# Optimization experiments

Hardware: AMD Instinct MI355X
Metric: run time of the kernel (lower is better)

## Reference

```python
import jax, jax.numpy as jnp
import numpy as np

NUM_POINTS = 1024  # K from init_kwargs


def setup_inputs() -> dict:
    key = jax.random.key(0)
    # [B, N, C]: xyz in channels 0:3, extra features (e.g. normals) in 3:6
    points = jax.random.normal(key, (16, 131072, 6), dtype=jnp.float32)
    return {"points": points}


def _fps_indices(xyz, K):
    """Iterative farthest-point sampling. xyz: [B, N, 3] -> idx [B, K] int32.
    random_start_point in the torch source is replaced by a fixed start (index 0)
    for determinism; the algorithm is otherwise identical."""
    B, N, _ = xyz.shape
    start = jnp.zeros((B,), dtype=jnp.int32)
    init_dists = jnp.full((B, N), jnp.inf, dtype=xyz.dtype)

    def step(carry, _):
        dists, last = carry
        # gather last selected point: [B, 1, 3]
        p = jnp.take_along_axis(xyz, last[:, None, None], axis=1)
        d = jnp.sum((xyz - p) ** 2, axis=-1)          # [B, N]
        dists = jnp.minimum(dists, d)                 # running min dist to selected set
        nxt = jnp.argmax(dists, axis=-1).astype(jnp.int32)
        return (dists, nxt), nxt

    (_, _), rest = jax.lax.scan(step, (init_dists, start), None, length=K - 1)
    # rest: [K-1, B] -> assemble [B, K] with the start index first
    idx = jnp.concatenate([start[:, None], rest.T], axis=1)
    return idx


def reference(points):
    xyz = points[:, :, :3].astype(jnp.float32)
    idx = _fps_indices(xyz, NUM_POINTS)               # [B, K]
    # masked_gather (all indices valid): gather rows along point dim
    out = jnp.take_along_axis(points, idx[:, :, None], axis=1)  # [B, K, C]
    return out
```

## Files before the change

### kernel.cpp

```cpp
#include <hip/hip_runtime.h>

#define BATCH 16
#define NPTS  131072
#define NCH   6
#define KSEL  1024
#define MBLK  16
#define TPB   256
#define CHUNK (NPTS / MBLK)
#define PPT   (CHUNK / TPB)
#define NWAVE (TPB / 64)
#define ROT   2


extern "C" __global__ __launch_bounds__(TPB)
void fps_kernel(const float* __restrict__ pts, float* __restrict__ out,
                unsigned long long* __restrict__ pub)
{
#pragma clang fp contract(off)
    __shared__ float              s_wd[NWAVE];
    __shared__ int                s_wi[NWAVE];
    __shared__ unsigned long long s_key[MBLK];

    const int b    = blockIdx.x % BATCH;
    const int m    = blockIdx.x / BATCH;
    const int tid  = threadIdx.x;
    const int base = m * CHUNK;
    const float* __restrict__ pb = pts + (size_t)b * NPTS * NCH;

    float xr[PPT], yr[PPT], zr[PPT], dmin[PPT];
#pragma unroll
    for (int i = 0; i < PPT; ++i) {
        const float* p = pb + (size_t)(base + tid + i * TPB) * NCH;
        xr[i]   = p[0];
        yr[i]   = p[1];
        zr[i]   = p[2];
        dmin[i] = __builtin_inff();
    }

    if (m == 0 && tid < NCH) out[(size_t)b * KSEL * NCH + tid] = pb[tid];

    float px = pb[0], py = pb[1], pz = pb[2];

    for (int k = 1; k < KSEL; ++k) {
        float bd = -1.0f;
        int   bj = 0;
#pragma unroll
        for (int i = 0; i < PPT; ++i) {
            float dx = __fsub_rn(xr[i], px);
            float dy = __fsub_rn(yr[i], py);
            float dz = __fsub_rn(zr[i], pz);
            float d  = __fadd_rn(__fadd_rn(__fmul_rn(dx, dx),
                                           __fmul_rn(dy, dy)),
                                 __fmul_rn(dz, dz));
            float dm = dmin[i];
            dm = (d < dm) ? d : dm;
            dmin[i] = dm;
            if (dm > bd) { bd = dm; bj = tid + i * TPB; }
        }

        for (int off = 32; off > 0; off >>= 1) {
            float od = __shfl_down(bd, off);
            int   oj = __shfl_down(bj, off);
            if (od > bd || (od == bd && oj < bj)) { bd = od; bj = oj; }
        }
        if ((tid & 63) == 0) {
            const int w = tid >> 6;
            s_wd[w] = bd; s_wi[w] = bj;
        }
        __syncthreads();

        unsigned long long* slot =
            pub + ((size_t)b * ROT + (size_t)(k & (ROT - 1))) * MBLK;

        if (tid == 0) {
            float fd = s_wd[0]; int fi = s_wi[0];
#pragma unroll
            for (int w = 1; w < NWAVE; ++w) {
                if (s_wd[w] > fd || (s_wd[w] == fd && s_wi[w] < fi)) {
                    fd = s_wd[w]; fi = s_wi[w];
                }
            }
            const unsigned g   = (unsigned)(base + fi);
            const unsigned inv = 0xFFFFFu ^ g;
            unsigned long long key =
                ((unsigned long long)__float_as_uint(fd) << 32)
                | ((unsigned long long)inv << 12)
                | (unsigned long long)(unsigned)k;
            __hip_atomic_store(&slot[m], key, __ATOMIC_RELAXED,
                               __HIP_MEMORY_SCOPE_AGENT);
        }

        if (tid < MBLK) {
            unsigned long long v;
            do {
                v = __hip_atomic_load(&slot[tid], __ATOMIC_RELAXED,
                                      __HIP_MEMORY_SCOPE_AGENT);
            } while ((unsigned)(v & 0xFFFull) != (unsigned)k);
            s_key[tid] = v;
        }
        __syncthreads();

        unsigned long long mx = s_key[0];
#pragma unroll
        for (int w = 1; w < MBLK; ++w) {
            if (s_key[w] > mx) mx = s_key[w];
        }
        const unsigned g = 0xFFFFFu ^ (unsigned)((mx >> 12) & 0xFFFFFull);
        const float* pp = pb + (size_t)g * NCH;
        px = pp[0]; py = pp[1]; pz = pp[2];

        if ((k & (MBLK - 1)) == m && tid == 0) {
            float* o = out + ((size_t)b * KSEL + k) * NCH;
#pragma unroll
            for (int c = 0; c < NCH; ++c) o[c] = pp[c];
        }
    }
}

extern "C" void kernel_launch(void* const* d_in, const int* in_sizes, int n_in,
                              void* d_out, int out_size, void* d_ws, size_t ws_size,
                              hipStream_t stream) {
    const float* pts = (const float*)d_in[0];
    float* out = (float*)d_out;
    unsigned long long* pub = (unsigned long long*)d_ws;

    hipMemsetAsync(d_ws, 0,
                   (size_t)BATCH * ROT * MBLK * sizeof(unsigned long long),
                   stream);

    void* args[] = { (void*)&pts, (void*)&out, (void*)&pub };
    hipLaunchCooperativeKernel((const void*)fps_kernel,
                               dim3(BATCH * MBLK), dim3(TPB),
                               args, 0, stream);
}
```

Measured before the change: 2.663 ms.

## Stream xyz from SoA workspace planes each iteration instead of holding in registers

Adds a COMPACT variant that writes the xyz coordinates into structure-of-arrays planes in the workspace, then reads them back as float4 loads from global/L2 on every iteration instead of keeping 32 points per thread in registers. Candidate point coordinates are also prefetched into shared memory by the polling threads, which removes the dependent global load after the argmax reduction. The aim is to lower register pressure and shorten the serial critical path. The cost is re-reading 1.5 MB per batch each iteration, and the variant is chosen only when the workspace is large enough.

```diff
diff --git a/kernel.cpp b/kernel.cpp
--- a/kernel.cpp
+++ b/kernel.cpp
@@ -10,9 +10,12 @@
 #define PPT   (CHUNK / TPB)
 #define NWAVE (TPB / 64)
 #define ROT   2
+#define PLANE_OFF 4096
+#define WS_NEED ((size_t)PLANE_OFF + 3ull * BATCH * NPTS * sizeof(float))
 
 
-extern "C" __global__ __launch_bounds__(TPB)
+template <int COMPACT>
+__global__ __launch_bounds__(TPB)
 void fps_kernel(const float* __restrict__ pts, float* __restrict__ out,
                 unsigned long long* __restrict__ pub)
 {
@@ -20,6 +23,7 @@
     __shared__ float              s_wd[NWAVE];
     __shared__ int                s_wi[NWAVE];
     __shared__ unsigned long long s_key[MBLK];
+    __shared__ float              s_cx[MBLK], s_cy[MBLK], s_cz[MBLK];
 
     const int b    = blockIdx.x % BATCH;
     const int m    = blockIdx.x / BATCH;
@@ -27,35 +31,82 @@
     const int base = m * CHUNK;
     const float* __restrict__ pb = pts + (size_t)b * NPTS * NCH;
 
-    float xr[PPT], yr[PPT], zr[PPT], dmin[PPT];
+    float* __restrict__ xp = (float*)((char*)pub + PLANE_OFF) + (size_t)b * NPTS;
+    float* __restrict__ yp = xp + (size_t)BATCH * NPTS;
+    float* __restrict__ zp = yp + (size_t)BATCH * NPTS;
+
+    float dmin[PPT];
 #pragma unroll
-    for (int i = 0; i < PPT; ++i) {
-        const float* p = pb + (size_t)(base + tid + i * TPB) * NCH;
-        xr[i]   = p[0];
-        yr[i]   = p[1];
-        zr[i]   = p[2];
-        dmin[i] = __builtin_inff();
+    for (int i = 0; i < PPT; ++i) dmin[i] = __builtin_inff();
+
+    float xr[PPT], yr[PPT], zr[PPT];
+
+    if (COMPACT) {
+#pragma unroll
+        for (int i = 0; i < PPT; ++i) {
+            const int j = base + tid + i * TPB;
+            const float* p = pb + (size_t)j * NCH;
+            xp[j] = p[0]; yp[j] = p[1]; zp[j] = p[2];
+        }
+    } else {
+#pragma unroll
+        for (int i = 0; i < PPT; ++i) {
+            const float* p = pb + (size_t)(base + tid + i * TPB) * NCH;
+            xr[i] = p[0]; yr[i] = p[1]; zr[i] = p[2];
+        }
     }
 
     if (m == 0 && tid < NCH) out[(size_t)b * KSEL * NCH + tid] = pb[tid];
+
+    if (COMPACT) { __threadfence(); }
+    __syncthreads();
+
+    const float4* __restrict__ xv = (const float4*)(xp + base + tid * PPT);
+    const float4* __restrict__ yv = (const float4*)(yp + base + tid * PPT);
+    const float4* __restrict__ zv = (const float4*)(zp + base + tid * PPT);
 
     float px = pb[0], py = pb[1], pz = pb[2];
 
     for (int k = 1; k < KSEL; ++k) {
         float bd = -1.0f;
         int   bj = 0;
+        if (COMPACT) {
 #pragma unroll
-        for (int i = 0; i < PPT; ++i) {
-            float dx = __fsub_rn(xr[i], px);
-            float dy = __fsub_rn(yr[i], py);
-            float dz = __fsub_rn(zr[i], pz);
-            float d  = __fadd_rn(__fadd_rn(__fmul_rn(dx, dx),
-                                           __fmul_rn(dy, dy)),
-                                 __fmul_rn(dz, dz));
-            float dm = dmin[i];
-            dm = (d < dm) ? d : dm;
-            dmin[i] = dm;
-            if (dm > bd) { bd = dm; bj = tid + i * TPB; }
+            for (int u = 0; u < PPT / 4; ++u) {
+                const float4 X = xv[u], Y = yv[u], Z = zv[u];
+#define FPS_DO(c, comp)                                                      \
+                {                                                            \
+                    float dx = __fsub_rn(X.comp, px);                        \
+                    float dy = __fsub_rn(Y.comp, py);                        \
+                    float dz = __fsub_rn(Z.comp, pz);                        \
+                    float d  = __fadd_rn(__fadd_rn(__fmul_rn(dx, dx),        \
+                                                   __fmul_rn(dy, dy)),       \
+                                         __fmul_rn(dz, dz));                 \
+                    const int i = u * 4 + (c);                               \
+                    float dm = dmin[i];                                      \
+                    dm = (d < dm) ? d : dm;                                  \
+                    dmin[i] = dm;                                            \
+                     \
+                                                            \
+                    if (dm > bd) { bd = dm; bj = tid * PPT + i; }            \
+                }
+                FPS_DO(0, x) FPS_DO(1, y) FPS_DO(2, z) FPS_DO(3, w)
+#undef FPS_DO
+            }
+        } else {
+#pragma unroll
+            for (int i = 0; i < PPT; ++i) {
+                float dx = __fsub_rn(xr[i], px);
+                float dy = __fsub_rn(yr[i], py);
+                float dz = __fsub_rn(zr[i], pz);
+                float d  = __fadd_rn(__fadd_rn(__fmul_rn(dx, dx),
+                                               __fmul_rn(dy, dy)),
+                                     __fmul_rn(dz, dz));
+                float dm = dmin[i];
+                dm = (d < dm) ? d : dm;
+                dmin[i] = dm;
+                if (dm > bd) { bd = dm; bj = tid + i * TPB; }
+            }
         }
 
         for (int off = 32; off > 0; off >>= 1) {
@@ -97,19 +148,28 @@
                                       __HIP_MEMORY_SCOPE_AGENT);
             } while ((unsigned)(v & 0xFFFull) != (unsigned)k);
             s_key[tid] = v;
+            const unsigned gw =
+                0xFFFFFu ^ (unsigned)((v >> 12) & 0xFFFFFull);
+            if (COMPACT) {
+                s_cx[tid] = xp[gw]; s_cy[tid] = yp[gw]; s_cz[tid] = zp[gw];
+            } else {
+                const float* cp = pb + (size_t)gw * NCH;
+                s_cx[tid] = cp[0]; s_cy[tid] = cp[1]; s_cz[tid] = cp[2];
+            }
         }
         __syncthreads();
 
-        unsigned long long mx = s_key[0];
+        unsigned long long mx = s_key[0]; int wsl = 0;
 #pragma unroll
         for (int w = 1; w < MBLK; ++w) {
-            if (s_key[w] > mx) mx = s_key[w];
+            if (s_key[w] > mx) { mx = s_key[w]; wsl = w; }
         }
-        const unsigned g = 0xFFFFFu ^ (unsigned)((mx >> 12) & 0xFFFFFull);
-        const float* pp = pb + (size_t)g * NCH;
-        px = pp[0]; py = pp[1]; pz = pp[2];
+        px = s_cx[wsl]; py = s_cy[wsl]; pz = s_cz[wsl];
 
         if ((k & (MBLK - 1)) == m && tid == 0) {
+            const unsigned g =
+                0xFFFFFu ^ (unsigned)((mx >> 12) & 0xFFFFFull);
+            const float* pp = pb + (size_t)g * NCH;
             float* o = out + ((size_t)b * KSEL + k) * NCH;
 #pragma unroll
             for (int c = 0; c < NCH; ++c) o[c] = pp[c];
@@ -129,7 +189,9 @@
                    stream);
 
     void* args[] = { (void*)&pts, (void*)&out, (void*)&pub };
-    hipLaunchCooperativeKernel((const void*)fps_kernel,
-                               dim3(BATCH * MBLK), dim3(TPB),
+    const void* fn = (ws_size >= WS_NEED)
+        ? (const void*)fps_kernel<1>
+        : (const void*)fps_kernel<0>;
+    hipLaunchCooperativeKernel(fn, dim3(BATCH * MBLK), dim3(TPB),
                                args, 0, stream);
 }
```

Result: slower. 6.810 ms (+155.7%).

## Poll partial maxima per wavefront with pipelined loads and drop second barrier

Applied to the files above, without the earlier changes.

Every wavefront now polls the 16 published per-block keys itself, keeping four relaxed atomic loads in flight, and reduces them with xor shuffles. This removes the second __syncthreads and the shared-memory staging of the cross-block keys. Per-wave candidates are packed into 64-bit keys before the block reduction, which simplifies the final compare. The cost is four times as many global polling loads, and each pipelined load may return a stale value.

```diff
diff --git a/kernel.cpp b/kernel.cpp
--- a/kernel.cpp
+++ b/kernel.cpp
@@ -17,13 +17,13 @@
                 unsigned long long* __restrict__ pub)
 {
 #pragma clang fp contract(off)
-    __shared__ float              s_wd[NWAVE];
-    __shared__ int                s_wi[NWAVE];
-    __shared__ unsigned long long s_key[MBLK];
+    __shared__ unsigned long long s_wkey[NWAVE];
 
     const int b    = blockIdx.x % BATCH;
     const int m    = blockIdx.x / BATCH;
     const int tid  = threadIdx.x;
+    const int wv   = tid >> 6;
+    const int lane = tid & 63;
     const int base = m * CHUNK;
     const float* __restrict__ pb = pts + (size_t)b * NPTS * NCH;
 
@@ -63,9 +63,14 @@
             int   oj = __shfl_down(bj, off);
             if (od > bd || (od == bd && oj < bj)) { bd = od; bj = oj; }
         }
-        if ((tid & 63) == 0) {
-            const int w = tid >> 6;
-            s_wd[w] = bd; s_wi[w] = bj;
+
+        if (lane == 0) {
+            const unsigned g   = (unsigned)(base + bj);
+            const unsigned inv = 0xFFFFFu ^ g;
+            s_wkey[wv] =
+                ((unsigned long long)__float_as_uint(bd) << 32)
+                | ((unsigned long long)inv << 12)
+                | (unsigned long long)(unsigned)k;
         }
         __syncthreads();
 
@@ -73,38 +78,40 @@
             pub + ((size_t)b * ROT + (size_t)(k & (ROT - 1))) * MBLK;
 
         if (tid == 0) {
-            float fd = s_wd[0]; int fi = s_wi[0];
+            unsigned long long kk = s_wkey[0];
 #pragma unroll
             for (int w = 1; w < NWAVE; ++w) {
-                if (s_wd[w] > fd || (s_wd[w] == fd && s_wi[w] < fi)) {
-                    fd = s_wd[w]; fi = s_wi[w];
-                }
+                if (s_wkey[w] > kk) kk = s_wkey[w];
             }
-            const unsigned g   = (unsigned)(base + fi);
-            const unsigned inv = 0xFFFFFu ^ g;
-            unsigned long long key =
-                ((unsigned long long)__float_as_uint(fd) << 32)
-                | ((unsigned long long)inv << 12)
-                | (unsigned long long)(unsigned)k;
-            __hip_atomic_store(&slot[m], key, __ATOMIC_RELAXED,
+            __hip_atomic_store(&slot[m], kk, __ATOMIC_RELAXED,
                                __HIP_MEMORY_SCOPE_AGENT);
         }
 
-        if (tid < MBLK) {
-            unsigned long long v;
-            do {
-                v = __hip_atomic_load(&slot[tid], __ATOMIC_RELAXED,
-                                      __HIP_MEMORY_SCOPE_AGENT);
-            } while ((unsigned)(v & 0xFFFull) != (unsigned)k);
-            s_key[tid] = v;
+        unsigned long long v = 0;
+        if (lane < MBLK) {
+            unsigned long long a0, a1, a2, a3;
+            a0 = __hip_atomic_load(&slot[lane], __ATOMIC_RELAXED,
+                                   __HIP_MEMORY_SCOPE_AGENT);
+            a1 = __hip_atomic_load(&slot[lane], __ATOMIC_RELAXED,
+                                   __HIP_MEMORY_SCOPE_AGENT);
+            a2 = __hip_atomic_load(&slot[lane], __ATOMIC_RELAXED,
+                                   __HIP_MEMORY_SCOPE_AGENT);
+            a3 = __hip_atomic_load(&slot[lane], __ATOMIC_RELAXED,
+                                   __HIP_MEMORY_SCOPE_AGENT);
+            for (;;) {
+                if ((unsigned)(a0 & 0xFFFull) == (unsigned)k) { v = a0; break; }
+                a0 = a1; a1 = a2; a2 = a3;
+                a3 = __hip_atomic_load(&slot[lane], __ATOMIC_RELAXED,
+                                       __HIP_MEMORY_SCOPE_AGENT);
+            }
         }
-        __syncthreads();
+#pragma unroll
+        for (int off = 8; off > 0; off >>= 1) {
+            unsigned long long o = __shfl_xor(v, off);
+            if (o > v) v = o;
+        }
+        const unsigned long long mx = __shfl(v, 0);
 
-        unsigned long long mx = s_key[0];
-#pragma unroll
-        for (int w = 1; w < MBLK; ++w) {
-            if (s_key[w] > mx) mx = s_key[w];
-        }
         const unsigned g = 0xFFFFFu ^ (unsigned)((mx >> 12) & 0xFFFFFull);
         const float* pp = pb + (size_t)g * NCH;
         px = pp[0]; py = pp[1]; pz = pp[2];
```

After: 4.518 ms. 69.6% more time.
